# Kernel tuning notes

Hardware: AMD Instinct MI355X
Metric: run time of the kernel (lower is better)

The kernel has to match this reference:

```python
import jax, jax.numpy as jnp
import numpy as np

EPS = 1e-6
B, T, D = 8, 4096, 512


def setup_inputs() -> dict:
    key = jax.random.key(0)
    ks = jax.random.split(key, 8)
    s = 1.0 / np.sqrt(D)
    return {
        "summarization": jax.random.normal(ks[0], (B, D), jnp.float32),
        "decoder_output": jax.random.normal(ks[1], (B, T, D), jnp.float32),
        "W_hist": jax.random.normal(ks[2], (D, D), jnp.float32) * s,
        "b_hist": jnp.zeros((D,), jnp.float32),
        "W1": jax.random.normal(ks[3], (D, D), jnp.float32) * s,
        "W2": jax.random.normal(ks[4], (D, D), jnp.float32) * s,
        "W_out": jax.random.normal(ks[5], (D, D), jnp.float32) * s,
        "b_out": jnp.zeros((D,), jnp.float32),
        "gamma": jnp.ones((D,), jnp.float32),
        "beta": jnp.zeros((D,), jnp.float32),
    }


def reference(summarization, decoder_output, W_hist, b_hist, W1, W2, W_out, b_out, gamma, beta):
    # Causal running mean: equivalent to tril-mask bmm / row-count, but O(T).
    tgt_len = decoder_output.shape[1]
    counts = jnp.arange(1, tgt_len + 1, dtype=decoder_output.dtype)[None, :, None]
    history = jnp.cumsum(decoder_output, axis=1) / counts            # [B,T,D]
    history = jnp.tanh(history @ W_hist + b_hist)                    # history_linear + tanh
    # TransformMinus: linear1(summ) - linear2(history), then linear_out + tanh
    summ_proj = (summarization @ W1)[:, None, :]                     # [B,1,D] broadcasts over T
    out = summ_proj - history @ W2
    future = jnp.tanh(out @ W_out + b_out)
    # LayerPostprocessing (eval: dropout = identity): LayerNorm(future + decoder_output)
    x = future + decoder_output
    mu = jnp.mean(x, axis=-1, keepdims=True)
    var = jnp.mean(jnp.square(x - mu), axis=-1, keepdims=True)
    return (x - mu) / jnp.sqrt(var + EPS) * gamma + beta
```

## Files before the change

### kernel.cpp

```cpp
#include <hip/hip_runtime.h>
#include <hip/hip_bf16.h>
#include <stdint.h>
#include <stddef.h>

#define DEV static __device__ __forceinline__

typedef __attribute__((ext_vector_type(8))) short short8;
typedef __attribute__((ext_vector_type(4))) float floatx4;

constexpr int Tn = 4096, Dn = 512;
constexpr int NC = 128, CTm = 32;

union U8s { uint4 u4; unsigned short us[8]; };
union U4f { float4 f4; float f[4]; };
union U4s { uint2 u2; unsigned short us[4]; };

DEV float b2f(unsigned short u) {
  union { unsigned int i; float f; } c; c.i = ((unsigned int)u) << 16; return c.f;
}
DEV unsigned short f2b(float f) {
  union { float f; unsigned int u; } c; c.f = f;
  unsigned int r = c.u + 0x7fffu + ((c.u >> 16) & 1u);
  return (unsigned short)(r >> 16);
}
DEV float fast_tanh(float x) {
  float e = __expf(2.0f * x);
  return 1.0f - 2.0f / (e + 1.0f);
}

typedef __attribute__((address_space(1))) void GVOID;
typedef __attribute__((address_space(3))) void LVOID;
DEV void async16(const unsigned short* g, unsigned short* l) {
  __builtin_amdgcn_global_load_lds((GVOID*)g, (LVOID*)l, 16, 0, 0);
}

__global__ void k_scan_partial(const float* __restrict__ dec, float* __restrict__ part) {
  int idx = blockIdx.x * 256 + threadIdx.x;
  int d4 = idx & 127;
  int c  = (idx >> 7) & (NC - 1);
  int b  = idx >> 14;
  const float* p = dec + ((size_t)b * Tn + (size_t)c * CTm) * Dn + d4 * 4;
  float s[4] = {0,0,0,0};
#pragma unroll 4
  for (int i = 0; i < CTm; ++i) {
    U4f v; v.f4 = *(const float4*)(p + (size_t)i * Dn);
#pragma unroll
    for (int j = 0; j < 4; ++j) s[j] += v.f[j];
  }
  float* o = part + ((size_t)(b * NC + c)) * Dn + d4 * 4;
#pragma unroll
  for (int j = 0; j < 4; ++j) o[j] = s[j];
}

__global__ void k_scan_apply(const float* __restrict__ dec,
                             const float* __restrict__ part,
                             unsigned short* __restrict__ M) {
  int idx = blockIdx.x * 256 + threadIdx.x;
  int d4 = idx & 127;
  int c  = (idx >> 7) & (NC - 1);
  int b  = idx >> 14;
  size_t rbase = (size_t)b * Tn + (size_t)c * CTm;
  U4f s; s.f4 = *(const float4*)(part + ((size_t)b * NC + c) * Dn + d4 * 4);
  int t0 = c * CTm;
  const float* dp = dec + rbase * Dn + d4 * 4;
  unsigned short* mp = M + rbase * Dn + d4 * 4;
#pragma unroll 4
  for (int i = 0; i < CTm; ++i) {
    U4f v; v.f4 = *(const float4*)(dp + (size_t)i * Dn);
    float inv = 1.0f / (float)(t0 + i + 1);
    U4s o;
#pragma unroll
    for (int j = 0; j < 4; ++j) { s.f[j] += v.f[j]; o.us[j] = f2b(s.f[j] * inv); }
    *(uint2*)(mp + (size_t)i * Dn) = o.u2;
  }
}

__global__ void k_svec(const float* __restrict__ summ,
                       const unsigned short* __restrict__ W1WoT,
                       const float* __restrict__ bo,
                       float* __restrict__ spo) {
  int widx = blockIdx.x * 4 + (threadIdx.x >> 6);
  int lane = threadIdx.x & 63;
  int n = widx & 511; int b = widx >> 9;
  U8s w8; w8.u4 = *(const uint4*)(W1WoT + (size_t)n * Dn + lane * 8);
  U4f s0, s1;
  s0.f4 = *(const float4*)(summ + (size_t)b * Dn + lane * 8);
  s1.f4 = *(const float4*)(summ + (size_t)b * Dn + lane * 8 + 4);
  float acc = 0.f;
#pragma unroll
  for (int j = 0; j < 4; ++j) acc += s0.f[j] * b2f(w8.us[j]);
#pragma unroll
  for (int j = 0; j < 4; ++j) acc += s1.f[j] * b2f(w8.us[j + 4]);
#pragma unroll
  for (int o = 32; o > 0; o >>= 1) acc += __shfl_xor(acc, o, 64);
  if (lane == 0) spo[(size_t)b * Dn + n] = acc + bo[n];
}

__global__ void k_wprep(const float* __restrict__ Wh, const float* __restrict__ Wo,
                        const float* __restrict__ W1, const float* __restrict__ W2,
                        unsigned short* __restrict__ WhT, unsigned short* __restrict__ WoT,
                        unsigned short* __restrict__ W1b, unsigned short* __restrict__ W2b,
                        float* __restrict__ part) {
  int blk = blockIdx.x;
  if (blk < 128) {
    const float* in = (blk < 64) ? Wh : Wo;
    unsigned short* out = (blk < 64) ? WhT : WoT;
    int lb = blk & 63;
    __shared__ float t[64][65];
    int n0 = (lb & 7) * 64, k0 = (lb >> 3) * 64;
#pragma unroll
    for (int l = 0; l < 16; ++l) {
      int lin = l * 256 + threadIdx.x;
      int r = lin >> 6, c = lin & 63;
      t[r][c] = in[(size_t)(k0 + r) * 512 + n0 + c];
    }
    __syncthreads();
#pragma unroll
    for (int l = 0; l < 16; ++l) {
      int lin = l * 256 + threadIdx.x;
      int r = lin >> 6, c = lin & 63;
      out[(size_t)(n0 + r) * 512 + k0 + c] = f2b(t[c][r]);
    }
  } else if (blk < 192) {
    const float* in = (blk < 160) ? W1 : W2;
    unsigned short* out = (blk < 160) ? W1b : W2b;
    int lb = (blk - 128) & 31;
    size_t base = ((size_t)lb * 256 + threadIdx.x) * 32;
#pragma unroll
    for (int l = 0; l < 8; ++l) {
      U4f v; v.f4 = *(const float4*)(in + base + l * 4);
      U4s o;
#pragma unroll
      for (int j = 0; j < 4; ++j) o.us[j] = f2b(v.f[j]);
      *(uint2*)(out + base + l * 4) = o.u2;
    }
  } else {
    int idx = (blk - 192) * 256 + threadIdx.x;
    int d4 = idx & 127;
    int b  = idx >> 7;
    float* p = part + (size_t)b * NC * Dn + d4 * 4;
    float s[4] = {0, 0, 0, 0};
    for (int c0 = 0; c0 < NC; c0 += 8) {
      U4f v[8];
#pragma unroll
      for (int i = 0; i < 8; ++i) v[i].f4 = *(const float4*)(p + (size_t)(c0 + i) * Dn);
#pragma unroll
      for (int i = 0; i < 8; ++i) {
        U4f o;
#pragma unroll
        for (int j = 0; j < 4; ++j) { o.f[j] = s[j]; s[j] += v[i].f[j]; }
        *(float4*)(p + (size_t)(c0 + i) * Dn) = o.f4;
      }
    }
  }
}

template<int EPI>
DEV void gemm_core(const unsigned short* __restrict__ A, const unsigned short* __restrict__ BT,
                   unsigned short* __restrict__ C, const float* __restrict__ bias,
                   const float* __restrict__ sproj, int m0, int n0) {
  __shared__ alignas(16) unsigned short sA[128 * 64];
  __shared__ alignas(16) unsigned short sB[128 * 64];
  const int tid  = threadIdx.x;
  const int lane = tid & 63;
  const int w    = tid >> 6;
  const int wm   = (w >> 1) * 64;
  const int wn   = (w & 1) * 64;
  const int rs   = lane & 15;
  const int quad = lane >> 4;

  floatx4 acc[4][4];
#pragma unroll
  for (int i = 0; i < 4; ++i)
#pragma unroll
    for (int j = 0; j < 4; ++j) acc[i][j] = (floatx4){0.f, 0.f, 0.f, 0.f};

  for (int kt = 0; kt < 512; kt += 64) {
#pragma unroll
    for (int l = 0; l < 4; ++l) {
      int ch = l * 256 + tid;
      int r = ch >> 3, kc = ch & 7;
      async16(A  + (size_t)(m0 + r) * 512 + kt + kc * 8, sA + (size_t)ch * 8);
      async16(BT + (size_t)(n0 + r) * 512 + kt + kc * 8, sB + (size_t)ch * 8);
    }
    asm volatile("s_waitcnt vmcnt(0)" ::: "memory");
    __syncthreads();

#pragma unroll
    for (int kk = 0; kk < 2; ++kk) {
      const int kb = kk * 32 + quad * 8;
      short8 af[4], bfr[4];
#pragma unroll
      for (int i = 0; i < 4; ++i)
        af[i] = *(const short8*)(sA + (size_t)(wm + i * 16 + rs) * 64 + kb);
#pragma unroll
      for (int j = 0; j < 4; ++j)
        bfr[j] = *(const short8*)(sB + (size_t)(wn + j * 16 + rs) * 64 + kb);
#pragma unroll
      for (int i = 0; i < 4; ++i)
#pragma unroll
        for (int j = 0; j < 4; ++j)
          acc[i][j] = __builtin_amdgcn_mfma_f32_16x16x32_bf16(af[i], bfr[j], acc[i][j], 0, 0, 0);
    }
    __syncthreads();
  }

#pragma unroll
  for (int i = 0; i < 4; ++i) {
#pragma unroll
    for (int j = 0; j < 4; ++j) {
      const int colg = n0 + wn + j * 16 + rs;
#pragma unroll
      for (int r = 0; r < 4; ++r) {
        const int rowg = m0 + wm + i * 16 + quad * 4 + r;
        float v = acc[i][j][r];
        if constexpr (EPI == 0)      v = fast_tanh(v + bias[colg]);
        else if constexpr (EPI == 3) v = fast_tanh(sproj[(rowg >> 12) * Dn + colg] - v);
        C[(size_t)rowg * 512 + colg] = f2b(v);
      }
    }
  }
}

template<int EPI>
__global__ __launch_bounds__(256, 2)
void k_gemm(const unsigned short* __restrict__ A, const unsigned short* __restrict__ BT,
            unsigned short* __restrict__ C, const float* __restrict__ bias,
            const float* __restrict__ sproj) {
  gemm_core<EPI>(A, BT, C, bias, sproj, blockIdx.x * 128, blockIdx.y * 128);
}

__global__ __launch_bounds__(256, 2)
void k_wgemm(const unsigned short* __restrict__ WoT,
             const unsigned short* __restrict__ W2b, const unsigned short* __restrict__ W1b,
             unsigned short* __restrict__ W2WoT, unsigned short* __restrict__ W1WoT) {
  const unsigned short* BT = blockIdx.z ? W1b : W2b;
  unsigned short* C = blockIdx.z ? W1WoT : W2WoT;
  gemm_core<2>(WoT, BT, C, nullptr, nullptr, blockIdx.x * 128, blockIdx.y * 128);
}

__global__ void k_ln(const unsigned short* __restrict__ F, const float* __restrict__ dec,
                     const float* __restrict__ gamma, const float* __restrict__ beta,
                     float* __restrict__ out) {
  int row  = blockIdx.x * 4 + (threadIdx.x >> 6);
  int lane = threadIdx.x & 63;
  size_t base = (size_t)row * Dn + lane * 8;
  U8s f8; f8.u4 = *(const uint4*)(F + base);
  U4f d0, d1; d0.f4 = *(const float4*)(dec + base); d1.f4 = *(const float4*)(dec + base + 4);
  float x[8]; float s = 0.f, sq = 0.f;
#pragma unroll
  for (int j = 0; j < 8; ++j) {
    float dv = (j < 4) ? d0.f[j] : d1.f[j - 4];
    x[j] = b2f(f8.us[j]) + dv; s += x[j]; sq += x[j] * x[j];
  }
#pragma unroll
  for (int o = 32; o > 0; o >>= 1) { s += __shfl_xor(s, o, 64); sq += __shfl_xor(sq, o, 64); }
  float mu   = s * (1.0f / 512.0f);
  float var  = sq * (1.0f / 512.0f) - mu * mu;
  float rstd = rsqrtf(var + 1e-6f);
  U4f g0, g1, b0, b1, o0, o1;
  g0.f4 = *(const float4*)(gamma + lane * 8); g1.f4 = *(const float4*)(gamma + lane * 8 + 4);
  b0.f4 = *(const float4*)(beta  + lane * 8); b1.f4 = *(const float4*)(beta  + lane * 8 + 4);
#pragma unroll
  for (int j = 0; j < 8; ++j) {
    float g = (j < 4) ? g0.f[j] : g1.f[j - 4];
    float b = (j < 4) ? b0.f[j] : b1.f[j - 4];
    float v = (x[j] - mu) * rstd * g + b;
    if (j < 4) o0.f[j] = v; else o1.f[j - 4] = v;
  }
  *(float4*)(out + base) = o0.f4;
  *(float4*)(out + base + 4) = o1.f4;
}

extern "C" void kernel_launch(void* const* d_in, const int* in_sizes, int n_in,
                              void* d_out, int out_size, void* d_ws, size_t ws_size,
                              hipStream_t stream) {
  (void)in_sizes; (void)n_in; (void)out_size; (void)ws_size;
  const float* summ = (const float*)d_in[0];
  const float* dec  = (const float*)d_in[1];
  const float* Wh   = (const float*)d_in[2];
  const float* bh   = (const float*)d_in[3];
  const float* W1   = (const float*)d_in[4];
  const float* W2   = (const float*)d_in[5];
  const float* Wo   = (const float*)d_in[6];
  const float* bo   = (const float*)d_in[7];
  const float* gam  = (const float*)d_in[8];
  const float* bet  = (const float*)d_in[9];
  float* out = (float*)d_out;

  char* ws = (char*)d_ws;
  unsigned short* Mbuf  = (unsigned short*)(ws);
  unsigned short* Hbuf  = (unsigned short*)(ws + 33554432);
  float*          part  = (float*)(ws + 67108864);
  float*          spo   = (float*)(ws + 69206016);
  unsigned short* WhT   = (unsigned short*)(ws + 69238784);
  unsigned short* WoT   = (unsigned short*)(ws + 69763072);
  unsigned short* W2b   = (unsigned short*)(ws + 70287360);
  unsigned short* W2WoT = (unsigned short*)(ws + 70811648);
  unsigned short* W1b   = (unsigned short*)(ws + 71335936);
  unsigned short* W1WoT = (unsigned short*)(ws + 71860224);

  k_scan_partial<<<512, 256, 0, stream>>>(dec, part);

  k_wprep<<<196, 256, 0, stream>>>(Wh, Wo, W1, W2, WhT, WoT, W1b, W2b, part);
  k_wgemm<<<dim3(4, 4, 2), 256, 0, stream>>>(WoT, W2b, W1b, W2WoT, W1WoT);

  k_svec<<<1024, 256, 0, stream>>>(summ, W1WoT, bo, spo);

  k_scan_apply<<<512, 256, 0, stream>>>(dec, part, Mbuf);

  k_gemm<0><<<dim3(256, 4), 256, 0, stream>>>(Mbuf, WhT, Hbuf, bh, nullptr);
  k_gemm<3><<<dim3(256, 4), 256, 0, stream>>>(Hbuf, W2WoT, Mbuf, nullptr, spo);

  k_ln<<<8192, 256, 0, stream>>>(Mbuf, dec, gam, bet, out);
}
```

Baseline: 244.2 us.

## Use 256x256 double-buffered swizzled GEMM tiles and merge small prep kernels

Replaces the 128x128 single-buffered bf16 MFMA GEMM with a 512-thread 256x256 tile. It double-buffers async global-to-LDS loads and XOR-swizzles the LDS layout to avoid bank conflicts, and raises wave priority around the MFMA section. This is meant to increase operand reuse and to overlap memory traffic with compute. The scan, weight prep, weight GEMM, prefix pass and summary-vector kernels are also merged into fewer launches to cut launch overhead. The trade-offs are a large LDS footprint (about 128KB per block), far fewer blocks in flight, and an 8-block weight GEMM that may serialise on few CUs.

```diff
diff --git a/kernel.cpp b/kernel.cpp
--- a/kernel.cpp
+++ b/kernel.cpp
@@ -34,108 +34,164 @@
   __builtin_amdgcn_global_load_lds((GVOID*)g, (LVOID*)l, 16, 0, 0);
 }
 
-__global__ void k_scan_partial(const float* __restrict__ dec, float* __restrict__ part) {
-  int idx = blockIdx.x * 256 + threadIdx.x;
-  int d4 = idx & 127;
-  int c  = (idx >> 7) & (NC - 1);
-  int b  = idx >> 14;
-  const float* p = dec + ((size_t)b * Tn + (size_t)c * CTm) * Dn + d4 * 4;
-  float s[4] = {0,0,0,0};
-#pragma unroll 4
-  for (int i = 0; i < CTm; ++i) {
-    U4f v; v.f4 = *(const float4*)(p + (size_t)i * Dn);
-#pragma unroll
-    for (int j = 0; j < 4; ++j) s[j] += v.f[j];
-  }
-  float* o = part + ((size_t)(b * NC + c)) * Dn + d4 * 4;
-#pragma unroll
-  for (int j = 0; j < 4; ++j) o[j] = s[j];
-}
-
-__global__ void k_scan_apply(const float* __restrict__ dec,
-                             const float* __restrict__ part,
-                             unsigned short* __restrict__ M) {
-  int idx = blockIdx.x * 256 + threadIdx.x;
-  int d4 = idx & 127;
-  int c  = (idx >> 7) & (NC - 1);
-  int b  = idx >> 14;
-  size_t rbase = (size_t)b * Tn + (size_t)c * CTm;
-  U4f s; s.f4 = *(const float4*)(part + ((size_t)b * NC + c) * Dn + d4 * 4);
-  int t0 = c * CTm;
-  const float* dp = dec + rbase * Dn + d4 * 4;
-  unsigned short* mp = M + rbase * Dn + d4 * 4;
-#pragma unroll 4
-  for (int i = 0; i < CTm; ++i) {
-    U4f v; v.f4 = *(const float4*)(dp + (size_t)i * Dn);
-    float inv = 1.0f / (float)(t0 + i + 1);
-    U4s o;
-#pragma unroll
-    for (int j = 0; j < 4; ++j) { s.f[j] += v.f[j]; o.us[j] = f2b(s.f[j] * inv); }
-    *(uint2*)(mp + (size_t)i * Dn) = o.u2;
-  }
-}
-
-__global__ void k_svec(const float* __restrict__ summ,
-                       const unsigned short* __restrict__ W1WoT,
-                       const float* __restrict__ bo,
-                       float* __restrict__ spo) {
-  int widx = blockIdx.x * 4 + (threadIdx.x >> 6);
-  int lane = threadIdx.x & 63;
-  int n = widx & 511; int b = widx >> 9;
-  U8s w8; w8.u4 = *(const uint4*)(W1WoT + (size_t)n * Dn + lane * 8);
-  U4f s0, s1;
-  s0.f4 = *(const float4*)(summ + (size_t)b * Dn + lane * 8);
-  s1.f4 = *(const float4*)(summ + (size_t)b * Dn + lane * 8 + 4);
-  float acc = 0.f;
-#pragma unroll
-  for (int j = 0; j < 4; ++j) acc += s0.f[j] * b2f(w8.us[j]);
-#pragma unroll
-  for (int j = 0; j < 4; ++j) acc += s1.f[j] * b2f(w8.us[j + 4]);
-#pragma unroll
-  for (int o = 32; o > 0; o >>= 1) acc += __shfl_xor(acc, o, 64);
-  if (lane == 0) spo[(size_t)b * Dn + n] = acc + bo[n];
-}
-
-__global__ void k_wprep(const float* __restrict__ Wh, const float* __restrict__ Wo,
+__global__ void k_fuse1(const float* __restrict__ dec, float* __restrict__ part,
+                        const float* __restrict__ Wh, const float* __restrict__ Wo,
                         const float* __restrict__ W1, const float* __restrict__ W2,
                         unsigned short* __restrict__ WhT, unsigned short* __restrict__ WoT,
-                        unsigned short* __restrict__ W1b, unsigned short* __restrict__ W2b,
-                        float* __restrict__ part) {
+                        unsigned short* __restrict__ W1b, unsigned short* __restrict__ W2b) {
   int blk = blockIdx.x;
-  if (blk < 128) {
-    const float* in = (blk < 64) ? Wh : Wo;
-    unsigned short* out = (blk < 64) ? WhT : WoT;
-    int lb = blk & 63;
-    __shared__ float t[64][65];
-    int n0 = (lb & 7) * 64, k0 = (lb >> 3) * 64;
-#pragma unroll
-    for (int l = 0; l < 16; ++l) {
-      int lin = l * 256 + threadIdx.x;
-      int r = lin >> 6, c = lin & 63;
-      t[r][c] = in[(size_t)(k0 + r) * 512 + n0 + c];
-    }
-    __syncthreads();
-#pragma unroll
-    for (int l = 0; l < 16; ++l) {
-      int lin = l * 256 + threadIdx.x;
-      int r = lin >> 6, c = lin & 63;
-      out[(size_t)(n0 + r) * 512 + k0 + c] = f2b(t[c][r]);
-    }
-  } else if (blk < 192) {
-    const float* in = (blk < 160) ? W1 : W2;
-    unsigned short* out = (blk < 160) ? W1b : W2b;
-    int lb = (blk - 128) & 31;
-    size_t base = ((size_t)lb * 256 + threadIdx.x) * 32;
-#pragma unroll
-    for (int l = 0; l < 8; ++l) {
-      U4f v; v.f4 = *(const float4*)(in + base + l * 4);
-      U4s o;
-#pragma unroll
-      for (int j = 0; j < 4; ++j) o.us[j] = f2b(v.f[j]);
-      *(uint2*)(out + base + l * 4) = o.u2;
-    }
+  if (blk < 512) {
+    int idx = blk * 256 + threadIdx.x;
+    int d4 = idx & 127;
+    int c  = (idx >> 7) & (NC - 1);
+    int b  = idx >> 14;
+    const float* p = dec + ((size_t)b * Tn + (size_t)c * CTm) * Dn + d4 * 4;
+    float s[4] = {0,0,0,0};
+#pragma unroll 4
+    for (int i = 0; i < CTm; ++i) {
+      U4f v; v.f4 = *(const float4*)(p + (size_t)i * Dn);
+#pragma unroll
+      for (int j = 0; j < 4; ++j) s[j] += v.f[j];
+    }
+    float* o = part + ((size_t)(b * NC + c)) * Dn + d4 * 4;
+#pragma unroll
+    for (int j = 0; j < 4; ++j) o[j] = s[j];
   } else {
-    int idx = (blk - 192) * 256 + threadIdx.x;
+    int wb = blk - 512;
+    if (wb < 128) {
+      const float* in = (wb < 64) ? Wh : Wo;
+      unsigned short* out = (wb < 64) ? WhT : WoT;
+      int lb = wb & 63;
+      __shared__ float t[64][65];
+      int n0 = (lb & 7) * 64, k0 = (lb >> 3) * 64;
+#pragma unroll
+      for (int l = 0; l < 16; ++l) {
+        int lin = l * 256 + threadIdx.x;
+        int r = lin >> 6, c = lin & 63;
+        t[r][c] = in[(size_t)(k0 + r) * 512 + n0 + c];
+      }
+      __syncthreads();
+#pragma unroll
+      for (int l = 0; l < 16; ++l) {
+        int lin = l * 256 + threadIdx.x;
+        int r = lin >> 6, c = lin & 63;
+        out[(size_t)(n0 + r) * 512 + k0 + c] = f2b(t[c][r]);
+      }
+    } else {
+      const float* in = (wb < 160) ? W1 : W2;
+      unsigned short* out = (wb < 160) ? W1b : W2b;
+      int lb = (wb - 128) & 31;
+      size_t base = ((size_t)lb * 256 + threadIdx.x) * 32;
+#pragma unroll
+      for (int l = 0; l < 8; ++l) {
+        U4f v; v.f4 = *(const float4*)(in + base + l * 4);
+        U4s o;
+#pragma unroll
+        for (int j = 0; j < 4; ++j) o.us[j] = f2b(v.f[j]);
+        *(uint2*)(out + base + l * 4) = o.u2;
+      }
+    }
+  }
+}
+
+template<int EPI>
+DEV void gemm256_core(const unsigned short* __restrict__ A, const unsigned short* __restrict__ BT,
+                      unsigned short* __restrict__ C, const float* __restrict__ bias,
+                      const float* __restrict__ sproj, int m0, int n0) {
+  __shared__ alignas(16) unsigned short sA[2][256 * 64];
+  __shared__ alignas(16) unsigned short sB[2][256 * 64];
+  const int tid  = threadIdx.x;
+  const int lane = tid & 63;
+  const int w    = tid >> 6;
+  const int wr   = w >> 2;
+  const int wc   = w & 3;
+  const int rs   = lane & 15;
+  const int quad = lane >> 4;
+
+  floatx4 acc[8][4];
+#pragma unroll
+  for (int i = 0; i < 8; ++i)
+#pragma unroll
+    for (int j = 0; j < 4; ++j) acc[i][j] = (floatx4){0.f, 0.f, 0.f, 0.f};
+
+  auto STAGE = [&](int kt, int buf) {
+#pragma unroll
+    for (int l = 0; l < 4; ++l) {
+      int ch = l * 512 + tid;
+      int r  = ch >> 3;
+      int kc = ((ch & 7) ^ (r & 7)) * 8;
+      async16(A  + (size_t)(m0 + r) * 512 + kt + kc, &sA[buf][ch * 8]);
+      async16(BT + (size_t)(n0 + r) * 512 + kt + kc, &sB[buf][ch * 8]);
+    }
+  };
+
+  auto COMPUTE = [&](int buf) {
+    __builtin_amdgcn_s_setprio(1);
+#pragma unroll
+    for (int kk = 0; kk < 2; ++kk) {
+      const int co = ((kk * 4 + quad) ^ (rs & 7)) * 8;
+      short8 bfr[4];
+#pragma unroll
+      for (int nj = 0; nj < 4; ++nj)
+        bfr[nj] = *(const short8*)(&sB[buf][(wc * 64 + nj * 16 + rs) * 64 + co]);
+#pragma unroll
+      for (int mi = 0; mi < 8; ++mi) {
+        short8 af = *(const short8*)(&sA[buf][(wr * 128 + mi * 16 + rs) * 64 + co]);
+#pragma unroll
+        for (int nj = 0; nj < 4; ++nj)
+          acc[mi][nj] = __builtin_amdgcn_mfma_f32_16x16x32_bf16(af, bfr[nj], acc[mi][nj], 0, 0, 0);
+      }
+    }
+    __builtin_amdgcn_s_setprio(0);
+  };
+
+  STAGE(0, 0);
+  for (int t = 0; t < 7; ++t) {
+    STAGE((t + 1) * 64, (t + 1) & 1);
+    asm volatile("s_waitcnt vmcnt(8)\n\ts_barrier" ::: "memory");
+    COMPUTE(t & 1);
+    asm volatile("s_barrier" ::: "memory");
+  }
+  asm volatile("s_waitcnt vmcnt(0)\n\ts_barrier" ::: "memory");
+  COMPUTE(1);
+
+#pragma unroll
+  for (int mi = 0; mi < 8; ++mi) {
+#pragma unroll
+    for (int nj = 0; nj < 4; ++nj) {
+      const int colg = n0 + wc * 64 + nj * 16 + rs;
+#pragma unroll
+      for (int r = 0; r < 4; ++r) {
+        const int rowg = m0 + wr * 128 + mi * 16 + quad * 4 + r;
+        float v = acc[mi][nj][r];
+        if constexpr (EPI == 0)      v = fast_tanh(v + bias[colg]);
+        else if constexpr (EPI == 3) v = fast_tanh(sproj[(rowg >> 12) * Dn + colg] - v);
+        C[(size_t)rowg * 512 + colg] = f2b(v);
+      }
+    }
+  }
+}
+
+template<int EPI>
+__global__ __launch_bounds__(512, 2)
+void k_gemm256(const unsigned short* __restrict__ A, const unsigned short* __restrict__ BT,
+               unsigned short* __restrict__ C, const float* __restrict__ bias,
+               const float* __restrict__ sproj) {
+  gemm256_core<EPI>(A, BT, C, bias, sproj, blockIdx.x * 256, blockIdx.y * 256);
+}
+
+__global__ __launch_bounds__(512, 2)
+void k_wgemm2(const unsigned short* __restrict__ WoT,
+              const unsigned short* __restrict__ W2b, const unsigned short* __restrict__ W1b,
+              unsigned short* __restrict__ W2WoT, unsigned short* __restrict__ W1WoT,
+              float* __restrict__ part) {
+  int blk = blockIdx.x;
+  if (blk < 8) {
+    const unsigned short* BT = (blk & 4) ? W1b : W2b;
+    unsigned short* Cc = (blk & 4) ? W1WoT : W2WoT;
+    gemm256_core<2>(WoT, BT, Cc, nullptr, nullptr, (blk & 1) * 256, ((blk >> 1) & 1) * 256);
+  } else {
+    int idx = (blk - 8) * 512 + threadIdx.x;
     int d4 = idx & 127;
     int b  = idx >> 7;
     float* p = part + (size_t)b * NC * Dn + d4 * 4;
@@ -155,88 +211,48 @@
   }
 }
 
-template<int EPI>
-DEV void gemm_core(const unsigned short* __restrict__ A, const unsigned short* __restrict__ BT,
-                   unsigned short* __restrict__ C, const float* __restrict__ bias,
-                   const float* __restrict__ sproj, int m0, int n0) {
-  __shared__ alignas(16) unsigned short sA[128 * 64];
-  __shared__ alignas(16) unsigned short sB[128 * 64];
-  const int tid  = threadIdx.x;
-  const int lane = tid & 63;
-  const int w    = tid >> 6;
-  const int wm   = (w >> 1) * 64;
-  const int wn   = (w & 1) * 64;
-  const int rs   = lane & 15;
-  const int quad = lane >> 4;
-
-  floatx4 acc[4][4];
-#pragma unroll
-  for (int i = 0; i < 4; ++i)
-#pragma unroll
-    for (int j = 0; j < 4; ++j) acc[i][j] = (floatx4){0.f, 0.f, 0.f, 0.f};
-
-  for (int kt = 0; kt < 512; kt += 64) {
-#pragma unroll
-    for (int l = 0; l < 4; ++l) {
-      int ch = l * 256 + tid;
-      int r = ch >> 3, kc = ch & 7;
-      async16(A  + (size_t)(m0 + r) * 512 + kt + kc * 8, sA + (size_t)ch * 8);
-      async16(BT + (size_t)(n0 + r) * 512 + kt + kc * 8, sB + (size_t)ch * 8);
-    }
-    asm volatile("s_waitcnt vmcnt(0)" ::: "memory");
-    __syncthreads();
-
-#pragma unroll
-    for (int kk = 0; kk < 2; ++kk) {
-      const int kb = kk * 32 + quad * 8;
-      short8 af[4], bfr[4];
-#pragma unroll
-      for (int i = 0; i < 4; ++i)
-        af[i] = *(const short8*)(sA + (size_t)(wm + i * 16 + rs) * 64 + kb);
-#pragma unroll
-      for (int j = 0; j < 4; ++j)
-        bfr[j] = *(const short8*)(sB + (size_t)(wn + j * 16 + rs) * 64 + kb);
-#pragma unroll
-      for (int i = 0; i < 4; ++i)
-#pragma unroll
-        for (int j = 0; j < 4; ++j)
-          acc[i][j] = __builtin_amdgcn_mfma_f32_16x16x32_bf16(af[i], bfr[j], acc[i][j], 0, 0, 0);
-    }
-    __syncthreads();
-  }
-
-#pragma unroll
-  for (int i = 0; i < 4; ++i) {
-#pragma unroll
-    for (int j = 0; j < 4; ++j) {
-      const int colg = n0 + wn + j * 16 + rs;
-#pragma unroll
-      for (int r = 0; r < 4; ++r) {
-        const int rowg = m0 + wm + i * 16 + quad * 4 + r;
-        float v = acc[i][j][r];
-        if constexpr (EPI == 0)      v = fast_tanh(v + bias[colg]);
-        else if constexpr (EPI == 3) v = fast_tanh(sproj[(rowg >> 12) * Dn + colg] - v);
-        C[(size_t)rowg * 512 + colg] = f2b(v);
-      }
-    }
-  }
-}
-
-template<int EPI>
-__global__ __launch_bounds__(256, 2)
-void k_gemm(const unsigned short* __restrict__ A, const unsigned short* __restrict__ BT,
-            unsigned short* __restrict__ C, const float* __restrict__ bias,
-            const float* __restrict__ sproj) {
-  gemm_core<EPI>(A, BT, C, bias, sproj, blockIdx.x * 128, blockIdx.y * 128);
-}
-
-__global__ __launch_bounds__(256, 2)
-void k_wgemm(const unsigned short* __restrict__ WoT,
-             const unsigned short* __restrict__ W2b, const unsigned short* __restrict__ W1b,
-             unsigned short* __restrict__ W2WoT, unsigned short* __restrict__ W1WoT) {
-  const unsigned short* BT = blockIdx.z ? W1b : W2b;
-  unsigned short* C = blockIdx.z ? W1WoT : W2WoT;
-  gemm_core<2>(WoT, BT, C, nullptr, nullptr, blockIdx.x * 128, blockIdx.y * 128);
+__global__ void k_fuse3(const float* __restrict__ dec, const float* __restrict__ part,
+                        unsigned short* __restrict__ M,
+                        const float* __restrict__ summ,
+                        const unsigned short* __restrict__ W1WoT,
+                        const float* __restrict__ bo, float* __restrict__ spo) {
+  int blk = blockIdx.x;
+  if (blk < 512) {
+    int idx = blk * 256 + threadIdx.x;
+    int d4 = idx & 127;
+    int c  = (idx >> 7) & (NC - 1);
+    int b  = idx >> 14;
+    size_t rbase = (size_t)b * Tn + (size_t)c * CTm;
+    U4f s; s.f4 = *(const float4*)(part + ((size_t)b * NC + c) * Dn + d4 * 4);
+    int t0 = c * CTm;
+    const float* dp = dec + rbase * Dn + d4 * 4;
+    unsigned short* mp = M + rbase * Dn + d4 * 4;
+#pragma unroll 4
+    for (int i = 0; i < CTm; ++i) {
+      U4f v; v.f4 = *(const float4*)(dp + (size_t)i * Dn);
+      float inv = 1.0f / (float)(t0 + i + 1);
+      U4s o;
+#pragma unroll
+      for (int j = 0; j < 4; ++j) { s.f[j] += v.f[j]; o.us[j] = f2b(s.f[j] * inv); }
+      *(uint2*)(mp + (size_t)i * Dn) = o.u2;
+    }
+  } else {
+    int widx = (blk - 512) * 4 + (threadIdx.x >> 6);
+    int lane = threadIdx.x & 63;
+    int n = widx & 511; int b = widx >> 9;
+    U8s w8; w8.u4 = *(const uint4*)(W1WoT + (size_t)n * Dn + lane * 8);
+    U4f s0, s1;
+    s0.f4 = *(const float4*)(summ + (size_t)b * Dn + lane * 8);
+    s1.f4 = *(const float4*)(summ + (size_t)b * Dn + lane * 8 + 4);
+    float acc = 0.f;
+#pragma unroll
+    for (int j = 0; j < 4; ++j) acc += s0.f[j] * b2f(w8.us[j]);
+#pragma unroll
+    for (int j = 0; j < 4; ++j) acc += s1.f[j] * b2f(w8.us[j + 4]);
+#pragma unroll
+    for (int o = 32; o > 0; o >>= 1) acc += __shfl_xor(acc, o, 64);
+    if (lane == 0) spo[(size_t)b * Dn + n] = acc + bo[n];
+  }
 }
 
 __global__ void k_ln(const unsigned short* __restrict__ F, const float* __restrict__ dec,
@@ -300,17 +316,14 @@
   unsigned short* W1b   = (unsigned short*)(ws + 71335936);
   unsigned short* W1WoT = (unsigned short*)(ws + 71860224);
 
-  k_scan_partial<<<512, 256, 0, stream>>>(dec, part);
-
-  k_wprep<<<196, 256, 0, stream>>>(Wh, Wo, W1, W2, WhT, WoT, W1b, W2b, part);
-  k_wgemm<<<dim3(4, 4, 2), 256, 0, stream>>>(WoT, W2b, W1b, W2WoT, W1WoT);
-
-  k_svec<<<1024, 256, 0, stream>>>(summ, W1WoT, bo, spo);
-
-  k_scan_apply<<<512, 256, 0, stream>>>(dec, part, Mbuf);
-
-  k_gemm<0><<<dim3(256, 4), 256, 0, stream>>>(Mbuf, WhT, Hbuf, bh, nullptr);
-  k_gemm<3><<<dim3(256, 4), 256, 0, stream>>>(Hbuf, W2WoT, Mbuf, nullptr, spo);
+  k_fuse1<<<704, 256, 0, stream>>>(dec, part, Wh, Wo, W1, W2, WhT, WoT, W1b, W2b);
+
+  k_wgemm2<<<10, 512, 0, stream>>>(WoT, W2b, W1b, W2WoT, W1WoT, part);
+
+  k_fuse3<<<1536, 256, 0, stream>>>(dec, part, Mbuf, summ, W1WoT, bo, spo);
+
+  k_gemm256<0><<<dim3(128, 2), 512, 0, stream>>>(Mbuf, WhT, Hbuf, bh, nullptr);
+  k_gemm256<3><<<dim3(128, 2), 512, 0, stream>>>(Hbuf, W2WoT, Mbuf, nullptr, spo);
 
   k_ln<<<8192, 256, 0, stream>>>(Mbuf, dec, gam, bet, out);
 }
```

New measurement: 238.5 us. 2.3% less time.
